# Optimization experiments

Hardware: AMD Instinct MI355X
Metric: run time of the kernel (lower is better)

Reference implementation:

```python
import jax, jax.numpy as jnp
import numpy as np

B, H, L, D = 4, 16, 8192, 64


def setup_inputs() -> dict:
    key = jax.random.key(0)
    ks = jax.random.split(key, 10)
    q = jax.random.normal(ks[0], (B, H, L, D), dtype=jnp.float32)
    k = jax.random.normal(ks[1], (B, H, L, D), dtype=jnp.float32)
    v = jax.random.normal(ks[2], (B, H, L, D), dtype=jnp.float32)
    mask = jax.random.randint(ks[3], (B, H, L), 0, 2, dtype=jnp.int32)
    s = 1.0 / np.sqrt(D)
    Wa_w = jax.random.uniform(ks[4], (D, D), jnp.float32, -s, s)  # torch Linear weight [out,in]
    Wa_b = jax.random.uniform(ks[5], (D,), jnp.float32, -s, s)
    Ua_w = jax.random.uniform(ks[6], (D, D), jnp.float32, -s, s)
    Ua_b = jax.random.uniform(ks[7], (D,), jnp.float32, -s, s)
    va_w = jax.random.uniform(ks[8], (1, D), jnp.float32, -s, s)
    va_b = jax.random.uniform(ks[9], (1,), jnp.float32, -s, s)
    return {"q": q, "k": k, "v": v, "mask": mask,
            "Wa_w": Wa_w, "Wa_b": Wa_b, "Ua_w": Ua_w, "Ua_b": Ua_b,
            "va_w": va_w, "va_b": va_b}


def reference(q, k, v, mask, Wa_w, Wa_b, Ua_w, Ua_b, va_w, va_b):
    # e1 = Wa(q), e2 = Ua(k)  (torch Linear: x @ W.T + b)
    e1 = jnp.einsum('bhld,ed->bhle', q, Wa_w) + Wa_b
    e2 = jnp.einsum('bhld,ed->bhle', k, Ua_w) + Ua_b
    t = jnp.tanh(e1 + e2)
    # va: [B,H,L,D] -> [B,H,L]
    e = jnp.einsum('bhld,d->bhl', t, va_w[0]) + va_b[0]
    e = jnp.where(mask == 0, jnp.float32(-10000.0), e)
    alpha = jax.nn.softmax(e, axis=-1)  # softmax over sequence length
    return alpha[..., None] * v
```

## Files before the change

kernel.cpp:

```cpp
#include <hip/hip_runtime.h>
#include <hip/hip_bf16.h>

#define BH   64
#define LSEQ 8192
#define DDIM 64
#define NPOS (BH * LSEQ)
#define NT4  (NPOS * DDIM / 4)

typedef __attribute__((ext_vector_type(8))) short bf16x8;
typedef __attribute__((ext_vector_type(4))) float f32x4;

__device__ inline short f2bf(float f) {
    __bf16 b = (__bf16)f;
    return __builtin_bit_cast(short, b);
}
__device__ inline float bf2f(short s) {
    unsigned u = ((unsigned)(unsigned short)s) << 16;
    return __builtin_bit_cast(float, u);
}
__device__ inline void split8(const float* f, bf16x8& hi, bf16x8& lo) {
#pragma unroll
    for (int j = 0; j < 8; j++) {
        short h = f2bf(f[j]);
        hi[j] = h;
        lo[j] = f2bf(f[j] - bf2f(h));
    }
}
__device__ inline float tanh_fast(float x) {
    float ex = __expf(2.f * x);
    return 1.f - 2.f * __builtin_amdgcn_rcpf(ex + 1.f);
}

__global__ __launch_bounds__(64, 2) void score_kernel(
    const float* __restrict__ q, const float* __restrict__ k,
    const int*   __restrict__ mask,
    const float* __restrict__ Waw, const float* __restrict__ Wab,
    const float* __restrict__ Uaw, const float* __restrict__ Uab,
    const float* __restrict__ vaw, const float* __restrict__ vab_p,
    float* __restrict__ e_out)
{
    const int lane = threadIdx.x;
    const int m    = lane & 15;
    const int g    = lane >> 4;
    const long t0  = (long)blockIdx.x * 4;

    __shared__ float lds[2][2048];

    bf16x8 bwa[4][2], bua[4][2];
    float bias_s[4], vav[4];
#pragma unroll
    for (int t = 0; t < 4; t++) {
        const int n = t * 16 + m;
        bias_s[t] = Wab[n] + Uab[n];
        vav[t]    = vaw[n];
#pragma unroll
        for (int s = 0; s < 2; s++) {
            const int k0 = s * 32 + g * 8;
            const float4 wA = ((const float4*)(Waw + n * 64 + k0))[0];
            const float4 wB = ((const float4*)(Waw + n * 64 + k0))[1];
            const float4 uA = ((const float4*)(Uaw + n * 64 + k0))[0];
            const float4 uB = ((const float4*)(Uaw + n * 64 + k0))[1];
            float wf[8] = {wA.x, wA.y, wA.z, wA.w, wB.x, wB.y, wB.z, wB.w};
            float uf[8] = {uA.x, uA.y, uA.z, uA.w, uB.x, uB.y, uB.z, uB.w};
            bf16x8 wv, uv;
#pragma unroll
            for (int j = 0; j < 8; j++) { wv[j] = f2bf(wf[j]); uv[j] = f2bf(uf[j]); }
            bwa[t][s] = wv;
            bua[t][s] = uv;
        }
    }
    const float vab = vab_p[0];
    const int4 mk0 = ((const int4*)mask)[(t0 + 0) * 4 + g];
    const int4 mk1 = ((const int4*)mask)[(t0 + 1) * 4 + g];
    const int4 mk2 = ((const int4*)mask)[(t0 + 2) * 4 + g];
    const int4 mk3 = ((const int4*)mask)[(t0 + 3) * 4 + g];

    auto issue_tile = [&](long tile, int buf) {
        const float* qb = q + tile * 1024;
        const float* kb = k + tile * 1024;
#pragma unroll
        for (int i = 0; i < 4; i++) {
            const int row = 4 * i + g;
            const int c   = m ^ (row & 7);
            __builtin_amdgcn_global_load_lds(
                (const __attribute__((address_space(1))) void*)(qb + row * 64 + c * 4),
                (__attribute__((address_space(3))) void*)(&lds[buf][i * 256]),
                16, 0, 0);
            __builtin_amdgcn_global_load_lds(
                (const __attribute__((address_space(1))) void*)(kb + row * 64 + c * 4),
                (__attribute__((address_space(3))) void*)(&lds[buf][1024 + i * 256]),
                16, 0, 0);
        }
    };

    auto compute = [&](int buf, const int4& mk, long tile) {
        f32x4 acc[4];
#pragma unroll
        for (int t = 0; t < 4; t++) acc[t] = (f32x4){0.f, 0.f, 0.f, 0.f};
        const float* L = lds[buf];
#pragma unroll
        for (int s = 0; s < 2; s++) {
            const int c0 = s * 8 + g * 2;
            const float4 qa = *((const float4*)(L + m * 64 + (( c0      ^ (m & 7)) << 2)));
            const float4 qb = *((const float4*)(L + m * 64 + (((c0 + 1) ^ (m & 7)) << 2)));
            const float4 ka = *((const float4*)(L + 1024 + m * 64 + (( c0      ^ (m & 7)) << 2)));
            const float4 kb = *((const float4*)(L + 1024 + m * 64 + (((c0 + 1) ^ (m & 7)) << 2)));
            float qf[8] = {qa.x, qa.y, qa.z, qa.w, qb.x, qb.y, qb.z, qb.w};
            float kf[8] = {ka.x, ka.y, ka.z, ka.w, kb.x, kb.y, kb.z, kb.w};
            bf16x8 qhi, qlo, khi, klo;
            split8(qf, qhi, qlo);
            split8(kf, khi, klo);
#pragma unroll
            for (int t = 0; t < 4; t++) {
                acc[t] = __builtin_amdgcn_mfma_f32_16x16x32_bf16(qhi, bwa[t][s], acc[t], 0, 0, 0);
                acc[t] = __builtin_amdgcn_mfma_f32_16x16x32_bf16(qlo, bwa[t][s], acc[t], 0, 0, 0);
                acc[t] = __builtin_amdgcn_mfma_f32_16x16x32_bf16(khi, bua[t][s], acc[t], 0, 0, 0);
                acc[t] = __builtin_amdgcn_mfma_f32_16x16x32_bf16(klo, bua[t][s], acc[t], 0, 0, 0);
            }
        }
        float c[4] = {0.f, 0.f, 0.f, 0.f};
#pragma unroll
        for (int t = 0; t < 4; t++) {
#pragma unroll
            for (int r = 0; r < 4; r++)
                c[r] += vav[t] * tanh_fast(acc[t][r] + bias_s[t]);
        }
#pragma unroll
        for (int r = 0; r < 4; r++) {
#pragma unroll
            for (int off2 = 1; off2 < 16; off2 <<= 1)
                c[r] += __shfl_xor(c[r], off2, 16);
        }
        if (m == 0) {
            float4 ev;
            ev.x = mk.x ? c[0] + vab : -10000.f;
            ev.y = mk.y ? c[1] + vab : -10000.f;
            ev.z = mk.z ? c[2] + vab : -10000.f;
            ev.w = mk.w ? c[3] + vab : -10000.f;
            *((float4*)(e_out + tile * 16 + g * 4)) = ev;
        }
    };

    issue_tile(t0 + 0, 0);
    issue_tile(t0 + 1, 1);
    asm volatile("s_waitcnt vmcnt(8)" ::: "memory");
    __builtin_amdgcn_sched_barrier(0);
    compute(0, mk0, t0 + 0);
    issue_tile(t0 + 2, 0);
    asm volatile("s_waitcnt vmcnt(9)" ::: "memory");
    __builtin_amdgcn_sched_barrier(0);
    compute(1, mk1, t0 + 1);
    issue_tile(t0 + 3, 1);
    asm volatile("s_waitcnt vmcnt(9)" ::: "memory");
    __builtin_amdgcn_sched_barrier(0);
    compute(0, mk2, t0 + 2);
    asm volatile("s_waitcnt vmcnt(1)" ::: "memory");
    __builtin_amdgcn_sched_barrier(0);
    compute(1, mk3, t0 + 3);
}

__global__ __launch_bounds__(1024) void rowstat_kernel(
    const float* __restrict__ e, float* __restrict__ stats)
{
    const int row = blockIdx.x;
    const size_t base = (size_t)row * LSEQ;
    const int tid  = threadIdx.x;
    const int lane = tid & 63;
    const int wv   = tid >> 6;
    __shared__ float redmax[16];
    __shared__ float redsum[16];

    float4 e0 = ((const float4*)(e + base))[tid];
    float4 e1 = ((const float4*)(e + base))[1024 + tid];
    float em[8] = {e0.x, e0.y, e0.z, e0.w, e1.x, e1.y, e1.z, e1.w};

    float lm = em[0];
#pragma unroll
    for (int j = 1; j < 8; j++) lm = fmaxf(lm, em[j]);
#pragma unroll
    for (int off = 32; off >= 1; off >>= 1) lm = fmaxf(lm, __shfl_xor(lm, off, 64));
    if (lane == 0) redmax[wv] = lm;
    __syncthreads();
    float M = redmax[0];
#pragma unroll
    for (int i = 1; i < 16; i++) M = fmaxf(M, redmax[i]);

    float ls = 0.f;
#pragma unroll
    for (int j = 0; j < 8; j++) ls += __expf(em[j] - M);
#pragma unroll
    for (int off = 32; off >= 1; off >>= 1) ls += __shfl_xor(ls, off, 64);
    if (lane == 0) redsum[wv] = ls;
    __syncthreads();
    if (tid == 0) {
        float S = 0.f;
#pragma unroll
        for (int i = 0; i < 16; i++) S += redsum[i];
        stats[row * 2]     = M;
        stats[row * 2 + 1] = 1.f / S;
    }
}

__global__ __launch_bounds__(256) void scale_kernel(
    const float* __restrict__ v, const float* __restrict__ e,
    const float* __restrict__ stats, float* __restrict__ out)
{
    const size_t b0 = (size_t)blockIdx.x * 1024 + threadIdx.x;
    const f32x4* vp = (const f32x4*)v;
    f32x4*       op = (f32x4*)out;

    size_t idx[4];
    f32x4  vv[4];
    float  ee[4];
    float2 st[4];
#pragma unroll
    for (int j = 0; j < 4; j++) {
        idx[j] = b0 + (size_t)j * 256;
        vv[j]  = __builtin_nontemporal_load(vp + idx[j]);
    }
#pragma unroll
    for (int j = 0; j < 4; j++) {
        const size_t p = idx[j] >> 4;
        ee[j] = e[p];
        st[j] = ((const float2*)stats)[p >> 13];
    }
#pragma unroll
    for (int j = 0; j < 4; j++) {
        const float a = __expf(ee[j] - st[j].x) * st[j].y;
        f32x4 o = vv[j] * a;
        __builtin_nontemporal_store(o, op + idx[j]);
    }
}

extern "C" void kernel_launch(void* const* d_in, const int* in_sizes, int n_in,
                              void* d_out, int out_size, void* d_ws, size_t ws_size,
                              hipStream_t stream) {
    const float* q    = (const float*)d_in[0];
    const float* k    = (const float*)d_in[1];
    const float* v    = (const float*)d_in[2];
    const int*   mask = (const int*)d_in[3];
    const float* Waw  = (const float*)d_in[4];
    const float* Wab  = (const float*)d_in[5];
    const float* Uaw  = (const float*)d_in[6];
    const float* Uab  = (const float*)d_in[7];
    const float* vaw  = (const float*)d_in[8];
    const float* vab  = (const float*)d_in[9];
    float* out = (float*)d_out;

    float* e_buf = (float*)d_ws;
    float* stats = (float*)d_ws + NPOS;

    score_kernel<<<NPOS / 64, 64, 0, stream>>>(q, k, mask, Waw, Wab, Uaw, Uab, vaw, vab, e_buf);
    rowstat_kernel<<<BH, 1024, 0, stream>>>(e_buf, stats);
    scale_kernel<<<NT4 / 1024, 256, 0, stream>>>(v, e_buf, stats, out);
}
```

Before: 414.3 us.

## Process more tiles per score block and defer masking to softmax kernels

The score kernel now loops over 16 tiles per block instead of 4 in a fixed double-buffered pipeline. This spreads the per-block weight conversion and register setup across more work and shrinks the grid. The mask loads move out of the score kernel: masked scores are replaced inside the row-statistics kernel, and the scale kernel writes zero for masked positions. The trade-off is extra mask reads in the two later kernels, and an all-masked row now gives zeros instead of a uniform distribution.

```diff
diff --git a/kernel.cpp b/kernel.cpp
--- a/kernel.cpp
+++ b/kernel.cpp
@@ -6,6 +6,7 @@
 #define DDIM 64
 #define NPOS (BH * LSEQ)
 #define NT4  (NPOS * DDIM / 4)
+#define TPB  16
 
 typedef __attribute__((ext_vector_type(8))) short bf16x8;
 typedef __attribute__((ext_vector_type(4))) float f32x4;
@@ -33,7 +34,6 @@
 
 __global__ __launch_bounds__(64, 2) void score_kernel(
     const float* __restrict__ q, const float* __restrict__ k,
-    const int*   __restrict__ mask,
     const float* __restrict__ Waw, const float* __restrict__ Wab,
     const float* __restrict__ Uaw, const float* __restrict__ Uab,
     const float* __restrict__ vaw, const float* __restrict__ vab_p,
@@ -42,7 +42,7 @@
     const int lane = threadIdx.x;
     const int m    = lane & 15;
     const int g    = lane >> 4;
-    const long t0  = (long)blockIdx.x * 4;
+    const long t0  = (long)blockIdx.x * TPB;
 
     __shared__ float lds[2][2048];
 
@@ -70,10 +70,6 @@
         }
     }
     const float vab = vab_p[0];
-    const int4 mk0 = ((const int4*)mask)[(t0 + 0) * 4 + g];
-    const int4 mk1 = ((const int4*)mask)[(t0 + 1) * 4 + g];
-    const int4 mk2 = ((const int4*)mask)[(t0 + 2) * 4 + g];
-    const int4 mk3 = ((const int4*)mask)[(t0 + 3) * 4 + g];
 
     auto issue_tile = [&](long tile, int buf) {
         const float* qb = q + tile * 1024;
@@ -93,7 +89,7 @@
         }
     };
 
-    auto compute = [&](int buf, const int4& mk, long tile) {
+    auto compute = [&](int buf, long tile) {
         f32x4 acc[4];
 #pragma unroll
         for (int t = 0; t < 4; t++) acc[t] = (f32x4){0.f, 0.f, 0.f, 0.f};
@@ -133,34 +129,42 @@
         }
         if (m == 0) {
             float4 ev;
-            ev.x = mk.x ? c[0] + vab : -10000.f;
-            ev.y = mk.y ? c[1] + vab : -10000.f;
-            ev.z = mk.z ? c[2] + vab : -10000.f;
-            ev.w = mk.w ? c[3] + vab : -10000.f;
+            ev.x = c[0] + vab;
+            ev.y = c[1] + vab;
+            ev.z = c[2] + vab;
+            ev.w = c[3] + vab;
             *((float4*)(e_out + tile * 16 + g * 4)) = ev;
         }
     };
+
+    asm volatile("s_waitcnt vmcnt(0)" ::: "memory");
+    __builtin_amdgcn_sched_barrier(0);
 
     issue_tile(t0 + 0, 0);
     issue_tile(t0 + 1, 1);
     asm volatile("s_waitcnt vmcnt(8)" ::: "memory");
     __builtin_amdgcn_sched_barrier(0);
-    compute(0, mk0, t0 + 0);
-    issue_tile(t0 + 2, 0);
-    asm volatile("s_waitcnt vmcnt(9)" ::: "memory");
-    __builtin_amdgcn_sched_barrier(0);
-    compute(1, mk1, t0 + 1);
-    issue_tile(t0 + 3, 1);
-    asm volatile("s_waitcnt vmcnt(9)" ::: "memory");
-    __builtin_amdgcn_sched_barrier(0);
-    compute(0, mk2, t0 + 2);
+#pragma unroll 1
+    for (int j = 0; j < TPB / 2 - 1; ++j) {
+        const long tb = t0 + 2 * j;
+        compute(0, tb + 0);
+        issue_tile(tb + 2, 0);
+        asm volatile("s_waitcnt vmcnt(9)" ::: "memory");
+        __builtin_amdgcn_sched_barrier(0);
+        compute(1, tb + 1);
+        issue_tile(tb + 3, 1);
+        asm volatile("s_waitcnt vmcnt(9)" ::: "memory");
+        __builtin_amdgcn_sched_barrier(0);
+    }
+    compute(0, t0 + TPB - 2);
     asm volatile("s_waitcnt vmcnt(1)" ::: "memory");
     __builtin_amdgcn_sched_barrier(0);
-    compute(1, mk3, t0 + 3);
+    compute(1, t0 + TPB - 1);
 }
 
 __global__ __launch_bounds__(1024) void rowstat_kernel(
-    const float* __restrict__ e, float* __restrict__ stats)
+    const float* __restrict__ e, const int* __restrict__ mask,
+    float* __restrict__ stats)
 {
     const int row = blockIdx.x;
     const size_t base = (size_t)row * LSEQ;
@@ -172,7 +176,12 @@
 
     float4 e0 = ((const float4*)(e + base))[tid];
     float4 e1 = ((const float4*)(e + base))[1024 + tid];
-    float em[8] = {e0.x, e0.y, e0.z, e0.w, e1.x, e1.y, e1.z, e1.w};
+    int4   m0 = ((const int4*)(mask + base))[tid];
+    int4   m1 = ((const int4*)(mask + base))[1024 + tid];
+    float em[8] = {m0.x ? e0.x : -10000.f, m0.y ? e0.y : -10000.f,
+                   m0.z ? e0.z : -10000.f, m0.w ? e0.w : -10000.f,
+                   m1.x ? e1.x : -10000.f, m1.y ? e1.y : -10000.f,
+                   m1.z ? e1.z : -10000.f, m1.w ? e1.w : -10000.f};
 
     float lm = em[0];
 #pragma unroll
@@ -203,6 +212,7 @@
 
 __global__ __launch_bounds__(256) void scale_kernel(
     const float* __restrict__ v, const float* __restrict__ e,
+    const int* __restrict__ mask,
     const float* __restrict__ stats, float* __restrict__ out)
 {
     const size_t b0 = (size_t)blockIdx.x * 1024 + threadIdx.x;
@@ -212,6 +222,7 @@
     size_t idx[4];
     f32x4  vv[4];
     float  ee[4];
+    int    mm[4];
     float2 st[4];
 #pragma unroll
     for (int j = 0; j < 4; j++) {
@@ -222,11 +233,12 @@
     for (int j = 0; j < 4; j++) {
         const size_t p = idx[j] >> 4;
         ee[j] = e[p];
+        mm[j] = mask[p];
         st[j] = ((const float2*)stats)[p >> 13];
     }
 #pragma unroll
     for (int j = 0; j < 4; j++) {
-        const float a = __expf(ee[j] - st[j].x) * st[j].y;
+        const float a = mm[j] ? __expf(ee[j] - st[j].x) * st[j].y : 0.f;
         f32x4 o = vv[j] * a;
         __builtin_nontemporal_store(o, op + idx[j]);
     }
@@ -250,7 +262,7 @@
     float* e_buf = (float*)d_ws;
     float* stats = (float*)d_ws + NPOS;
 
-    score_kernel<<<NPOS / 64, 64, 0, stream>>>(q, k, mask, Waw, Wab, Uaw, Uab, vaw, vab, e_buf);
-    rowstat_kernel<<<BH, 1024, 0, stream>>>(e_buf, stats);
-    scale_kernel<<<NT4 / 1024, 256, 0, stream>>>(v, e_buf, stats, out);
-}
+    score_kernel<<<NPOS / (16 * TPB), 64, 0, stream>>>(q, k, Waw, Wab, Uaw, Uab, vaw, vab, e_buf);
+    rowstat_kernel<<<BH, 1024, 0, stream>>>(e_buf, mask, stats);
+    scale_kernel<<<NT4 / 1024, 256, 0, stream>>>(v, e_buf, mask, stats, out);
+}
```

Measured after the change: 418.6 us. Within noise of the previous version (+1.0%).
